# Kernel tuning notes

Hardware: AMD Instinct MI355X
Metric: run time of the kernel (lower is better)

Reference implementation:

```python
import jax, jax.numpy as jnp
import numpy as np

V, E, H = 50000, 300, 256  # vocab, word dim, per-direction hidden (nfeat_sent=2H=512)
B, T = 256, 64
NEG = -1e9


def _lstm_scan(x, mask, w_ih, w_hh, b):
    """x: [T,B,E], mask: [T,B,1] float. Masked steps keep (h,c) unchanged.
    Gate order matches torch.nn.LSTM: i, f, g, o."""
    Bsz = x.shape[1]
    Hd = w_hh.shape[1]
    init = (jnp.zeros((Bsz, Hd), x.dtype), jnp.zeros((Bsz, Hd), x.dtype))

    def step(carry, inp):
        h, c = carry
        xt, mt = inp
        z = xt @ w_ih.T + h @ w_hh.T + b  # [B,4H]
        i, f, g, o = jnp.split(z, 4, axis=-1)
        i = jax.nn.sigmoid(i); f = jax.nn.sigmoid(f)
        g = jnp.tanh(g); o = jax.nn.sigmoid(o)
        c_new = f * c + i * g
        h_new = o * jnp.tanh(c_new)
        c = mt * c_new + (1.0 - mt) * c
        h = mt * h_new + (1.0 - mt) * h
        return (h, c), h

    _, hs = jax.lax.scan(step, init, (x, mask))
    return hs  # [T,B,H]


def setup_inputs() -> dict:
    key = jax.random.key(0)
    ks = jax.random.split(key, 9)
    token_ids = jax.random.randint(ks[0], (B, T), 0, V, dtype=jnp.int32)
    lengths = jax.random.randint(ks[1], (B,), 1, T + 1, dtype=jnp.int32)
    emb = jax.random.normal(ks[2], (V, E), jnp.float32) * 0.1
    s = 0.05
    w_ih_f = jax.random.normal(ks[3], (4 * H, E), jnp.float32) * s
    w_hh_f = jax.random.normal(ks[4], (4 * H, H), jnp.float32) * s
    b_f = jax.random.normal(ks[5], (4 * H,), jnp.float32) * s  # b_ih + b_hh fused
    w_ih_b = jax.random.normal(ks[6], (4 * H, E), jnp.float32) * s
    w_hh_b = jax.random.normal(ks[7], (4 * H, H), jnp.float32) * s
    b_b = jax.random.normal(ks[8], (4 * H,), jnp.float32) * s
    return {"token_ids": token_ids, "lengths": lengths, "emb": emb,
            "w_ih_f": w_ih_f, "w_hh_f": w_hh_f, "b_f": b_f,
            "w_ih_b": w_ih_b, "w_hh_b": w_hh_b, "b_b": b_b}


def reference(token_ids, lengths, emb, w_ih_f, w_hh_f, b_f, w_ih_b, w_hh_b, b_b):
    # Batched equivalent of the per-sentence loop: embed -> biLSTM -> max over time.
    x = emb[token_ids]                              # [B,T,E]
    x = jnp.swapaxes(x, 0, 1)                       # [T,B,E] (time-major)
    valid = (jnp.arange(T)[:, None] < lengths[None, :])  # [T,B]
    mask = valid.astype(x.dtype)[:, :, None]        # [T,B,1]

    h_fwd = _lstm_scan(x, mask, w_ih_f, w_hh_f, b_f)  # [T,B,H]
    # Backward direction: reverse time; masked (pad) steps leave state at zero,
    # so each sentence's backward pass starts exactly at its last real token.
    h_bwd = _lstm_scan(x[::-1], mask[::-1], w_ih_b, w_hh_b, b_b)[::-1]

    out = jnp.concatenate([h_fwd, h_bwd], axis=-1)  # [T,B,2H]
    out = jnp.where(valid[:, :, None], out, NEG)
    return jnp.max(out, axis=0)                     # [B, 2H] == [B, nfeat_sent]
```

## Files before the change

kernel.cpp:

```cpp
#include <hip/hip_runtime.h>
#include <hip/hip_bf16.h>
#include <math.h>

#define VV 50000
#define EE 300
#define HD 256
#define BB 256
#define TT 64
#define NEGV -1e9f

#define OFF_H    0
#define OFF_C    262144
#define OFF_CTR  262144
#define OFF_B2   393216
#define OFF_WHHF 395264
#define OFF_WIHF 919552
#define WS_FULL_BYTES (1247232ULL * 4ULL)

typedef __attribute__((ext_vector_type(8))) short bf16x8;
typedef __attribute__((ext_vector_type(4))) float f32x4;

__device__ __forceinline__ float sigf(float x) {
  return 1.f / (1.f + __expf(-x));
}
__device__ __forceinline__ float tanhfast(float x) {
  return 1.f - 2.f / (__expf(2.f * x) + 1.f);
}
__device__ __forceinline__ unsigned short f2bf(float f) {
  union { float f; unsigned u; } x;
  x.f = f;
  unsigned r = x.u + 0x7fffu + ((x.u >> 16) & 1u);
  return (unsigned short)(r >> 16);
}

__global__ __launch_bounds__(256) void prep_all(
    const float* __restrict__ whf, const float* __restrict__ whb,
    const float* __restrict__ wif, const float* __restrict__ wib,
    const float* __restrict__ bf, const float* __restrict__ bb,
    float* __restrict__ ws) {
  int idx = blockIdx.x * 256 + threadIdx.x;
  if (idx < 131072) ws[OFF_H + idx] = 0.f;
  if (idx < 2048) {
    ((unsigned int*)(ws + OFF_CTR))[idx] = 0u;
    int dir = idx >> 10, jg = idx & 1023, j = jg >> 2, g = jg & 3;
    ws[OFF_B2 + idx] = (dir ? bb : bf)[g * HD + j];
  }
  if (idx < 65536) {
    int lane = idx & 63, kt = (idx >> 6) & 7, ngrp = (idx >> 9) & 63,
        dir = idx >> 15;
    int n = ngrp * 16 + (lane & 15);
    int j = n >> 2, g = n & 3;
    int k0 = kt * 32 + (lane >> 4) * 8;
    const float* W = dir ? whb : whf;
    const float* src = W + (size_t)((g << 8) + j) * HD + k0;
    union { unsigned short u[8]; uint4 q; } hp, lp;
#pragma unroll
    for (int e = 0; e < 8; ++e) {
      float v = src[e];
      unsigned short hh = f2bf(v);
      union { unsigned u; float f; } hf;
      hf.u = (unsigned)hh << 16;
      hp.u[e] = hh;
      lp.u[e] = f2bf(v - hf.f);
    }
    unsigned short* dst = (unsigned short*)(ws + OFF_WHHF) + (size_t)idx * 16;
    *(uint4*)dst = hp.q;
    *(uint4*)(dst + 8) = lp.q;
  }
  if (idx < 81920) {
    int lane = idx & 63;
    int f = idx >> 6;
    int kt = f % 10;
    int ngrp = (f / 10) & 63;
    int dir = f / 640;
    int n = ngrp * 16 + (lane & 15);
    int j = n >> 2, g = n & 3;
    int k0 = kt * 32 + (lane >> 4) * 8;
    const float* W = dir ? wib : wif;
    union { unsigned short u[8]; uint4 q; } p;
#pragma unroll
    for (int e = 0; e < 8; ++e) {
      int k = k0 + e;
      p.u[e] = (k < EE) ? f2bf(W[(size_t)((g << 8) + j) * EE + k])
                        : (unsigned short)0;
    }
    *(uint4*)((unsigned short*)(ws + OFF_WIHF) + (size_t)idx * 8) = p.q;
  }
}

__global__ __launch_bounds__(256) void init_kernel(float* __restrict__ ws,
                                                   float* __restrict__ out) {
  int idx = blockIdx.x * 256 + threadIdx.x;
  if (idx < 393216) ws[idx] = 0.f;
  if (idx < BB * 2 * HD) out[idx] = NEGV;
}

__global__ __launch_bounds__(512) void lstm_persist(
    const int* __restrict__ tok, const int* __restrict__ lens,
    const float* __restrict__ emb, float* __restrict__ ws,
    float* __restrict__ out) {
  const int bg = blockIdx.x;
  const int slice = blockIdx.y;
  const int dir = blockIdx.z;
  const int tid = threadIdx.x;
  const int lane = tid & 63;
  const int wv = tid >> 6;

  __shared__ __align__(16) unsigned short hfr[8192];
  __shared__ __align__(16) unsigned short ebuf[2][5120];
  __shared__ float z_sm[16][132];

  bf16x8 whi[8], wlo[8], wih[10];
  {
    const int ngrp = slice * 8 + wv;
    const unsigned short* p = (const unsigned short*)(ws + OFF_WHHF) +
                              (size_t)(((dir * 64 + ngrp) * 8) * 64 + lane) * 16;
#pragma unroll
    for (int kt = 0; kt < 8; ++kt) {
      whi[kt] = *(const bf16x8*)(p + kt * 1024);
      wlo[kt] = *(const bf16x8*)(p + kt * 1024 + 8);
    }
    const unsigned short* q = (const unsigned short*)(ws + OFF_WIHF) +
                              (size_t)(((dir * 64 + ngrp) * 10) * 64 + lane) * 8;
#pragma unroll
    for (int kt = 0; kt < 10; ++kt) wih[kt] = *(const bf16x8*)(q + kt * 512);
  }

  const int rg = tid >> 5;
  const int k8 = tid & 31;
  const int jl = tid & 31;
  const int brow = bg * 16 + rg;
  const int len = lens[brow];
  const int j = slice * 32 + jl;
  const float4 bias =
      *(const float4*)(ws + OFF_B2 + dir * 1024 + slice * 128 + jl * 4);
  unsigned int* ctr =
      (unsigned int*)(ws + OFF_CTR) + (size_t)(dir * 16 + bg) * 32;
  float* hb = ws + OFF_H;
  const int ld_r = lane & 15, ld_oct = lane >> 4;
  const int trow = brow * TT;
  const int o2 = 32 + (k8 & 7);
  const bool has2 = (k8 < 8);
  const int slot1 = (k8 >> 2) * 64 + rg * 4 + (k8 & 3);
  const int slot2 = ((o2 >> 2) * 64) + rg * 4 + (o2 & 3);

  float c = 0.f, omax = NEGV, h_prev = 0.f;

  {
    const int t0 = dir ? (TT - 1) : 0;
    const float* er = emb + (size_t)tok[trow + t0] * EE;
    float4 a0 = *(const float4*)(er + k8 * 8);
    float4 a1 = *(const float4*)(er + k8 * 8 + 4);
    union { unsigned short u[8]; uint4 q; } p;
    p.u[0] = f2bf(a0.x); p.u[1] = f2bf(a0.y); p.u[2] = f2bf(a0.z);
    p.u[3] = f2bf(a0.w); p.u[4] = f2bf(a1.x); p.u[5] = f2bf(a1.y);
    p.u[6] = f2bf(a1.z); p.u[7] = f2bf(a1.w);
    *(uint4*)&ebuf[0][slot1 * 8] = p.q;
    if (has2) {
      float4 b0 = make_float4(0.f, 0.f, 0.f, 0.f);
      float4 b1 = make_float4(0.f, 0.f, 0.f, 0.f);
      if (o2 <= 37) b0 = *(const float4*)(er + o2 * 8);
      if (o2 < 37) b1 = *(const float4*)(er + o2 * 8 + 4);
      union { unsigned short u[8]; uint4 q; } p2;
      p2.u[0] = f2bf(b0.x); p2.u[1] = f2bf(b0.y); p2.u[2] = f2bf(b0.z);
      p2.u[3] = f2bf(b0.w); p2.u[4] = f2bf(b1.x); p2.u[5] = f2bf(b1.y);
      p2.u[6] = f2bf(b1.z); p2.u[7] = f2bf(b1.w);
      *(uint4*)&ebuf[0][slot2 * 8] = p2.q;
    }
  }

  for (int s = 0; s < TT; ++s) {
    const int t = dir ? (TT - 1 - s) : s;
    const bool nstage = (s < TT - 1);
    const unsigned long long* s8 = (const unsigned long long*)(
        hb + (size_t)(((s & 1) * 2 + dir) * 256 + brow) * 256 + k8 * 8);
    unsigned long long u0 =
        __hip_atomic_load(s8 + 0, __ATOMIC_RELAXED, __HIP_MEMORY_SCOPE_AGENT);
    unsigned long long u1 =
        __hip_atomic_load(s8 + 1, __ATOMIC_RELAXED, __HIP_MEMORY_SCOPE_AGENT);
    unsigned long long u2 =
        __hip_atomic_load(s8 + 2, __ATOMIC_RELAXED, __HIP_MEMORY_SCOPE_AGENT);
    unsigned long long u3 =
        __hip_atomic_load(s8 + 3, __ATOMIC_RELAXED, __HIP_MEMORY_SCOPE_AGENT);
    float4 pe0, pe1, qe0, qe1;
    if (nstage) {
      const int tn = dir ? (TT - 2 - s) : (s + 1);
      const float* er = emb + (size_t)tok[trow + tn] * EE;
      pe0 = *(const float4*)(er + k8 * 8);
      pe1 = *(const float4*)(er + k8 * 8 + 4);
      qe0 = make_float4(0.f, 0.f, 0.f, 0.f);
      qe1 = make_float4(0.f, 0.f, 0.f, 0.f);
      if (has2) {
        if (o2 <= 37) qe0 = *(const float4*)(er + o2 * 8);
        if (o2 < 37) qe1 = *(const float4*)(er + o2 * 8 + 4);
      }
    }
    {
      float v[8];
      __builtin_memcpy(&v[0], &u0, 8);
      __builtin_memcpy(&v[2], &u1, 8);
      __builtin_memcpy(&v[4], &u2, 8);
      __builtin_memcpy(&v[6], &u3, 8);
      union { unsigned short u[8]; uint4 q; } hp, lp;
#pragma unroll
      for (int e = 0; e < 8; ++e) {
        unsigned short hh = f2bf(v[e]);
        union { unsigned u; float f; } hf;
        hf.u = (unsigned)hh << 16;
        hp.u[e] = hh;
        lp.u[e] = f2bf(v[e] - hf.f);
      }
      *(uint4*)&hfr[slot1 * 8] = hp.q;
      *(uint4*)&hfr[4096 + slot1 * 8] = lp.q;
    }
    __syncthreads();
    f32x4 acc[4];
#pragma unroll
    for (int i = 0; i < 4; ++i) {
      acc[i][0] = 0.f; acc[i][1] = 0.f; acc[i][2] = 0.f; acc[i][3] = 0.f;
    }
    const unsigned short* eb = ebuf[s & 1];
#pragma unroll
    for (int kt = 0; kt < 10; ++kt) {
      bf16x8 ax = *(const bf16x8*)(eb + (kt * 64 + ld_r * 4 + ld_oct) * 8);
      acc[kt & 3] =
          __builtin_amdgcn_mfma_f32_16x16x32_bf16(ax, wih[kt], acc[kt & 3], 0, 0, 0);
    }
#pragma unroll
    for (int kt = 0; kt < 8; ++kt) {
      const int sl = (kt * 64 + ld_r * 4 + ld_oct) * 8;
      bf16x8 ahi = *(const bf16x8*)(hfr + sl);
      bf16x8 alo = *(const bf16x8*)(hfr + 4096 + sl);
      f32x4 a = acc[kt & 3];
      a = __builtin_amdgcn_mfma_f32_16x16x32_bf16(ahi, whi[kt], a, 0, 0, 0);
      a = __builtin_amdgcn_mfma_f32_16x16x32_bf16(alo, whi[kt], a, 0, 0, 0);
      a = __builtin_amdgcn_mfma_f32_16x16x32_bf16(ahi, wlo[kt], a, 0, 0, 0);
      acc[kt & 3] = a;
    }
    f32x4 zf = (acc[0] + acc[1]) + (acc[2] + acc[3]);
#pragma unroll
    for (int i = 0; i < 4; ++i)
      z_sm[ld_oct * 4 + i][wv * 16 + ld_r] = zf[i];
    __syncthreads();
    const float4 z4 = *(const float4*)&z_sm[rg][jl * 4];
    float h_out = h_prev;
    if (t < len) {
      float ig = sigf(z4.x + bias.x);
      float fg = sigf(z4.y + bias.y);
      float gg = tanhfast(z4.z + bias.z);
      float og = sigf(z4.w + bias.w);
      c = fg * c + ig * gg;
      float hn = og * tanhfast(c);
      h_out = hn;
      omax = fmaxf(omax, hn);
    }
    h_prev = h_out;
    if (nstage) {
      float* dst =
          hb + (size_t)(((((s + 1) & 1) * 2 + dir) * 256) + brow) * 256 + j;
      __hip_atomic_store(dst, h_out, __ATOMIC_RELAXED,
                         __HIP_MEMORY_SCOPE_AGENT);
      unsigned short* ebn = ebuf[(s + 1) & 1];
      {
        union { unsigned short u[8]; uint4 q; } p;
        p.u[0] = f2bf(pe0.x); p.u[1] = f2bf(pe0.y); p.u[2] = f2bf(pe0.z);
        p.u[3] = f2bf(pe0.w); p.u[4] = f2bf(pe1.x); p.u[5] = f2bf(pe1.y);
        p.u[6] = f2bf(pe1.z); p.u[7] = f2bf(pe1.w);
        *(uint4*)&ebn[slot1 * 8] = p.q;
        if (has2) {
          union { unsigned short u[8]; uint4 q; } p2;
          p2.u[0] = f2bf(qe0.x); p2.u[1] = f2bf(qe0.y); p2.u[2] = f2bf(qe0.z);
          p2.u[3] = f2bf(qe0.w); p2.u[4] = f2bf(qe1.x); p2.u[5] = f2bf(qe1.y);
          p2.u[6] = f2bf(qe1.z); p2.u[7] = f2bf(qe1.w);
          *(uint4*)&ebn[slot2 * 8] = p2.q;
        }
      }
      asm volatile("s_waitcnt vmcnt(0)" ::: "memory");
      __syncthreads();
      if (tid == 0) {
        __hip_atomic_fetch_add(ctr, 1u, __ATOMIC_RELAXED,
                               __HIP_MEMORY_SCOPE_AGENT);
      }
      if (tid < 64) {
        const unsigned int target = 8u * (unsigned)(s + 1);
        while (__hip_atomic_load(ctr, __ATOMIC_RELAXED,
                                 __HIP_MEMORY_SCOPE_AGENT) < target) {
        }
      }
      __syncthreads();
      asm volatile("" ::: "memory");
    }
  }
  out[(size_t)brow * (2 * HD) + dir * HD + j] = omax;
}

__global__ __launch_bounds__(256) void step_fused(
    const int* __restrict__ tok, const int* __restrict__ lens,
    const float* __restrict__ emb,
    const float* __restrict__ wih_f, const float* __restrict__ whh_f,
    const float* __restrict__ bias_f,
    const float* __restrict__ wih_b, const float* __restrict__ whh_b,
    const float* __restrict__ bias_b,
    float* __restrict__ ws, float* __restrict__ out, int s) {
  const int tid = threadIdx.x;
  const int jt = blockIdx.x, bt = blockIdx.y, dir = blockIdx.z;
  const int j0 = jt * 32, b0g = bt * 16;
  const int t = (dir == 0) ? s : (TT - 1 - s);
  const float* Wih = dir ? wih_b : wih_f;
  const float* Whh = dir ? whh_b : whh_f;
  const float* bias = dir ? bias_b : bias_f;
  const float* hcur = ws + OFF_H + (size_t)((s & 1) * 2 + dir) * BB * HD;
  float* hnxt = ws + OFF_H + (size_t)(((s + 1) & 1) * 2 + dir) * BB * HD;
  float* cbuf = ws + OFF_C + (size_t)dir * BB * HD;

  __shared__ float a_sm[16][64];
  __shared__ float w_sm[64][132];
  __shared__ float z_sm[16][132];

  const int cg = tid & 31, bg = tid >> 5;
  float acc[2][4] = {{0.f, 0.f, 0.f, 0.f}, {0.f, 0.f, 0.f, 0.f}};

  for (int phase = 0; phase < 2; ++phase) {
    const float* W = phase ? Whh : Wih;
    const int K = phase ? HD : EE;
    for (int k0 = 0; k0 < K; k0 += 64) {
      const int klen = (K - k0) < 64 ? (K - k0) : 64;
      {
        int bl = tid >> 4, kk4 = tid & 15;
        if (kk4 * 4 < klen) {
          const float* src;
          if (phase == 0) {
            int tk = tok[(b0g + bl) * TT + t];
            src = emb + (size_t)tk * EE + k0 + kk4 * 4;
          } else {
            src = hcur + (size_t)(b0g + bl) * HD + k0 + kk4 * 4;
          }
          *(float4*)&a_sm[bl][kk4 * 4] = *(const float4*)src;
        }
      }
      for (int i = 0; i < 8; ++i) {
        int e = i * 256 + tid;
        int col = e >> 4, kk4 = e & 15;
        if (kk4 * 4 < klen) {
          int gcol = ((col >> 5) * HD) + j0 + (col & 31);
          float4 v = *(const float4*)(W + (size_t)gcol * K + k0 + kk4 * 4);
          w_sm[kk4 * 4 + 0][col] = v.x;
          w_sm[kk4 * 4 + 1][col] = v.y;
          w_sm[kk4 * 4 + 2][col] = v.z;
          w_sm[kk4 * 4 + 3][col] = v.w;
        }
      }
      __syncthreads();
      for (int k = 0; k < klen; ++k) {
        float a0 = a_sm[bg * 2 + 0][k];
        float a1 = a_sm[bg * 2 + 1][k];
        float4 w = *(const float4*)&w_sm[k][cg * 4];
        acc[0][0] += a0 * w.x; acc[0][1] += a0 * w.y;
        acc[0][2] += a0 * w.z; acc[0][3] += a0 * w.w;
        acc[1][0] += a1 * w.x; acc[1][1] += a1 * w.y;
        acc[1][2] += a1 * w.z; acc[1][3] += a1 * w.w;
      }
      __syncthreads();
    }
  }
  *(float4*)&z_sm[bg * 2 + 0][cg * 4] =
      make_float4(acc[0][0], acc[0][1], acc[0][2], acc[0][3]);
  *(float4*)&z_sm[bg * 2 + 1][cg * 4] =
      make_float4(acc[1][0], acc[1][1], acc[1][2], acc[1][3]);
  __syncthreads();
  for (int pi = 0; pi < 2; ++pi) {
    int p = pi * 256 + tid;
    int bl = p >> 5, jl = p & 31;
    int bglob = b0g + bl, jglob = j0 + jl;
    bool valid = t < lens[bglob];
    float h_old = hcur[(size_t)bglob * HD + jglob];
    float h_out = h_old;
    if (valid) {
      float zi = z_sm[bl][0 + jl] + bias[0 * HD + jglob];
      float zf = z_sm[bl][32 + jl] + bias[1 * HD + jglob];
      float zg = z_sm[bl][64 + jl] + bias[2 * HD + jglob];
      float zo = z_sm[bl][96 + jl] + bias[3 * HD + jglob];
      float ig = sigf(zi), fg = sigf(zf), gg = tanhf(zg), og = sigf(zo);
      float c_old = cbuf[(size_t)bglob * HD + jglob];
      float c_new = fg * c_old + ig * gg;
      float h_new = og * tanhf(c_new);
      cbuf[(size_t)bglob * HD + jglob] = c_new;
      h_out = h_new;
      float* op = out + (size_t)bglob * (2 * HD) + dir * HD + jglob;
      *op = fmaxf(*op, h_new);
    }
    hnxt[(size_t)bglob * HD + jglob] = h_out;
  }
}

extern "C" void kernel_launch(void* const* d_in, const int* in_sizes, int n_in,
                              void* d_out, int out_size, void* d_ws,
                              size_t ws_size, hipStream_t stream) {
  const int* tok = (const int*)d_in[0];
  const int* lens = (const int*)d_in[1];
  const float* emb = (const float*)d_in[2];
  const float* wih_f = (const float*)d_in[3];
  const float* whh_f = (const float*)d_in[4];
  const float* b_f = (const float*)d_in[5];
  const float* wih_b = (const float*)d_in[6];
  const float* whh_b = (const float*)d_in[7];
  const float* b_b = (const float*)d_in[8];
  float* out = (float*)d_out;
  float* ws = (float*)d_ws;

  const bool full = ws_size >= WS_FULL_BYTES;
  if (full) {
    hipLaunchKernelGGL(prep_all, dim3(512), dim3(256), 0, stream, whh_f,
                       whh_b, wih_f, wih_b, b_f, b_b, ws);
    hipLaunchKernelGGL(lstm_persist, dim3(16, 8, 2), dim3(512), 0, stream,
                       tok, lens, emb, ws, out);
  } else {
    hipLaunchKernelGGL(init_kernel, dim3(1536), dim3(256), 0, stream, ws, out);
    for (int s = 0; s < TT; ++s) {
      hipLaunchKernelGGL(step_fused, dim3(8, 16, 2), dim3(256), 0, stream, tok,
                         lens, emb, wih_f, whh_f, b_f, wih_b, whh_b, b_b, ws,
                         out, s);
    }
  }
}
```

Measured before the change: 220.3 us.

## Exchange hidden state as pre-split bf16 fragments and replace LDS gate transpose with shuffles

The producer now writes the hidden state to global memory already split into bf16 hi/lo pairs in the MFMA fragment layout. Consumers can copy it straight into LDS without per-step conversion. The gate results are regrouped across lanes with xor-shuffles instead of a z_sm shared-memory round trip, which removes one __syncthreads per step. The cost is two 16-bit scattered atomic stores per element instead of one float store, plus a larger workspace layout.

```diff
diff --git a/kernel.cpp b/kernel.cpp
--- a/kernel.cpp
+++ b/kernel.cpp
@@ -9,13 +9,14 @@
 #define TT 64
 #define NEGV -1e9f
 
-#define OFF_H    0
-#define OFF_C    262144
-#define OFF_CTR  262144
-#define OFF_B2   393216
-#define OFF_WHHF 395264
-#define OFF_WIHF 919552
-#define WS_FULL_BYTES (1247232ULL * 4ULL)
+#define OFF_HF   0
+#define OFF_CTR  524288
+#define OFF_B2   526336
+#define OFF_WHHF 528384
+#define OFF_WIHF 1052672
+#define WS_FULL_BYTES (1380352ULL * 4ULL)
+#define FB_H 0
+#define FB_C 262144
 
 typedef __attribute__((ext_vector_type(8))) short bf16x8;
 typedef __attribute__((ext_vector_type(4))) float f32x4;
@@ -39,7 +40,7 @@
     const float* __restrict__ bf, const float* __restrict__ bb,
     float* __restrict__ ws) {
   int idx = blockIdx.x * 256 + threadIdx.x;
-  if (idx < 131072) ws[OFF_H + idx] = 0.f;
+  if (idx < 131072) ws[OFF_HF + idx] = 0.f;
   if (idx < 2048) {
     ((unsigned int*)(ws + OFF_CTR))[idx] = 0u;
     int dir = idx >> 10, jg = idx & 1023, j = jg >> 2, g = jg & 3;
@@ -106,13 +107,12 @@
   const int lane = tid & 63;
   const int wv = tid >> 6;
 
-  __shared__ __align__(16) unsigned short hfr[8192];
+  __shared__ __align__(16) unsigned short hfr[2][512][8];
   __shared__ __align__(16) unsigned short ebuf[2][5120];
-  __shared__ float z_sm[16][132];
 
   bf16x8 whi[8], wlo[8], wih[10];
+  const int ngrp = slice * 8 + wv;
   {
-    const int ngrp = slice * 8 + wv;
     const unsigned short* p = (const unsigned short*)(ws + OFF_WHHF) +
                               (size_t)(((dir * 64 + ngrp) * 8) * 64 + lane) * 16;
 #pragma unroll
@@ -128,27 +128,35 @@
 
   const int rg = tid >> 5;
   const int k8 = tid & 31;
-  const int jl = tid & 31;
-  const int brow = bg * 16 + rg;
-  const int len = lens[brow];
-  const int j = slice * 32 + jl;
-  const float4 bias =
-      *(const float4*)(ws + OFF_B2 + dir * 1024 + slice * 128 + jl * 4);
-  unsigned int* ctr =
-      (unsigned int*)(ws + OFF_CTR) + (size_t)(dir * 16 + bg) * 32;
-  float* hb = ws + OFF_H;
-  const int ld_r = lane & 15, ld_oct = lane >> 4;
-  const int trow = brow * TT;
+  const int stage_row = bg * 16 + rg;
+  const int strow = stage_row * TT;
   const int o2 = 32 + (k8 & 7);
   const bool has2 = (k8 < 8);
   const int slot1 = (k8 >> 2) * 64 + rg * 4 + (k8 & 3);
   const int slot2 = ((o2 >> 2) * 64) + rg * 4 + (o2 & 3);
 
+  const int q = lane & 3;
+  const int base = lane & 12;
+  const int r = (lane >> 4) * 4 + q;
+  const int gate_row = bg * 16 + r;
+  const int len = lens[gate_row];
+  const int jloc = ngrp * 4 + (base >> 2);
+  const float4 bias4 =
+      *(const float4*)(ws + OFF_B2 + dir * 1024 + ngrp * 16 + base);
+  const int slot_j = (jloc >> 5) * 64 + r * 4 + ((jloc >> 3) & 3);
+  const int e_j = jloc & 7;
+
+  const int ld_slot = (lane & 15) * 4 + (lane >> 4);
+
+  unsigned int* ctr =
+      (unsigned int*)(ws + OFF_CTR) + (size_t)(dir * 16 + bg) * 32;
+  unsigned short* hfg = (unsigned short*)(ws + OFF_HF);
+
   float c = 0.f, omax = NEGV, h_prev = 0.f;
 
   {
     const int t0 = dir ? (TT - 1) : 0;
-    const float* er = emb + (size_t)tok[trow + t0] * EE;
+    const float* er = emb + (size_t)tok[strow + t0] * EE;
     float4 a0 = *(const float4*)(er + k8 * 8);
     float4 a1 = *(const float4*)(er + k8 * 8 + 4);
     union { unsigned short u[8]; uint4 q; } p;
@@ -172,20 +180,24 @@
   for (int s = 0; s < TT; ++s) {
     const int t = dir ? (TT - 1 - s) : s;
     const bool nstage = (s < TT - 1);
-    const unsigned long long* s8 = (const unsigned long long*)(
-        hb + (size_t)(((s & 1) * 2 + dir) * 256 + brow) * 256 + k8 * 8);
-    unsigned long long u0 =
-        __hip_atomic_load(s8 + 0, __ATOMIC_RELAXED, __HIP_MEMORY_SCOPE_AGENT);
-    unsigned long long u1 =
-        __hip_atomic_load(s8 + 1, __ATOMIC_RELAXED, __HIP_MEMORY_SCOPE_AGENT);
-    unsigned long long u2 =
-        __hip_atomic_load(s8 + 2, __ATOMIC_RELAXED, __HIP_MEMORY_SCOPE_AGENT);
-    unsigned long long u3 =
-        __hip_atomic_load(s8 + 3, __ATOMIC_RELAXED, __HIP_MEMORY_SCOPE_AGENT);
+    const unsigned long long* hsrc = (const unsigned long long*)(
+        hfg + (size_t)(((s & 1) * 2 + dir) * 16 + bg) * 8192);
+    unsigned long long hu0 = __hip_atomic_load(hsrc + tid * 4 + 0,
+                                               __ATOMIC_RELAXED,
+                                               __HIP_MEMORY_SCOPE_AGENT);
+    unsigned long long hu1 = __hip_atomic_load(hsrc + tid * 4 + 1,
+                                               __ATOMIC_RELAXED,
+                                               __HIP_MEMORY_SCOPE_AGENT);
+    unsigned long long hu2 = __hip_atomic_load(hsrc + tid * 4 + 2,
+                                               __ATOMIC_RELAXED,
+                                               __HIP_MEMORY_SCOPE_AGENT);
+    unsigned long long hu3 = __hip_atomic_load(hsrc + tid * 4 + 3,
+                                               __ATOMIC_RELAXED,
+                                               __HIP_MEMORY_SCOPE_AGENT);
     float4 pe0, pe1, qe0, qe1;
     if (nstage) {
       const int tn = dir ? (TT - 2 - s) : (s + 1);
-      const float* er = emb + (size_t)tok[trow + tn] * EE;
+      const float* er = emb + (size_t)tok[strow + tn] * EE;
       pe0 = *(const float4*)(er + k8 * 8);
       pe1 = *(const float4*)(er + k8 * 8 + 4);
       qe0 = make_float4(0.f, 0.f, 0.f, 0.f);
@@ -196,22 +208,11 @@
       }
     }
     {
-      float v[8];
-      __builtin_memcpy(&v[0], &u0, 8);
-      __builtin_memcpy(&v[2], &u1, 8);
-      __builtin_memcpy(&v[4], &u2, 8);
-      __builtin_memcpy(&v[6], &u3, 8);
-      union { unsigned short u[8]; uint4 q; } hp, lp;
-#pragma unroll
-      for (int e = 0; e < 8; ++e) {
-        unsigned short hh = f2bf(v[e]);
-        union { unsigned u; float f; } hf;
-        hf.u = (unsigned)hh << 16;
-        hp.u[e] = hh;
-        lp.u[e] = f2bf(v[e] - hf.f);
-      }
-      *(uint4*)&hfr[slot1 * 8] = hp.q;
-      *(uint4*)&hfr[4096 + slot1 * 8] = lp.q;
+      unsigned long long* hdst_l = (unsigned long long*)hfr;
+      hdst_l[tid * 4 + 0] = hu0;
+      hdst_l[tid * 4 + 1] = hu1;
+      hdst_l[tid * 4 + 2] = hu2;
+      hdst_l[tid * 4 + 3] = hu3;
     }
     __syncthreads();
     f32x4 acc[4];
@@ -222,15 +223,14 @@
     const unsigned short* eb = ebuf[s & 1];
 #pragma unroll
     for (int kt = 0; kt < 10; ++kt) {
-      bf16x8 ax = *(const bf16x8*)(eb + (kt * 64 + ld_r * 4 + ld_oct) * 8);
+      bf16x8 ax = *(const bf16x8*)(eb + (kt * 64 + ld_slot) * 8);
       acc[kt & 3] =
           __builtin_amdgcn_mfma_f32_16x16x32_bf16(ax, wih[kt], acc[kt & 3], 0, 0, 0);
     }
 #pragma unroll
     for (int kt = 0; kt < 8; ++kt) {
-      const int sl = (kt * 64 + ld_r * 4 + ld_oct) * 8;
-      bf16x8 ahi = *(const bf16x8*)(hfr + sl);
-      bf16x8 alo = *(const bf16x8*)(hfr + 4096 + sl);
+      bf16x8 ahi = *(const bf16x8*)&hfr[0][kt * 64 + ld_slot][0];
+      bf16x8 alo = *(const bf16x8*)&hfr[1][kt * 64 + ld_slot][0];
       f32x4 a = acc[kt & 3];
       a = __builtin_amdgcn_mfma_f32_16x16x32_bf16(ahi, whi[kt], a, 0, 0, 0);
       a = __builtin_amdgcn_mfma_f32_16x16x32_bf16(alo, whi[kt], a, 0, 0, 0);
@@ -238,17 +238,29 @@
       acc[kt & 3] = a;
     }
     f32x4 zf = (acc[0] + acc[1]) + (acc[2] + acc[3]);
-#pragma unroll
-    for (int i = 0; i < 4; ++i)
-      z_sm[ld_oct * 4 + i][wv * 16 + ld_r] = zf[i];
-    __syncthreads();
-    const float4 z4 = *(const float4*)&z_sm[rg][jl * 4];
+    float v0 = zf[0], v1 = zf[1], v2 = zf[2], v3 = zf[3];
+    {
+      float s0 = __shfl_xor(v1, 1), s1 = __shfl_xor(v0, 1);
+      float s2 = __shfl_xor(v3, 1), s3 = __shfl_xor(v2, 1);
+      const bool qb = (q & 1) != 0;
+      float a0 = qb ? s0 : v0;
+      float a1 = qb ? v1 : s1;
+      float a2 = qb ? s2 : v2;
+      float a3 = qb ? v3 : s3;
+      float t0 = __shfl_xor(a2, 2), t1 = __shfl_xor(a3, 2);
+      float t2 = __shfl_xor(a0, 2), t3 = __shfl_xor(a1, 2);
+      const bool q2 = (q & 2) != 0;
+      v0 = q2 ? t0 : a0;
+      v1 = q2 ? t1 : a1;
+      v2 = q2 ? a2 : t2;
+      v3 = q2 ? a3 : t3;
+    }
     float h_out = h_prev;
     if (t < len) {
-      float ig = sigf(z4.x + bias.x);
-      float fg = sigf(z4.y + bias.y);
-      float gg = tanhfast(z4.z + bias.z);
-      float og = sigf(z4.w + bias.w);
+      float ig = sigf(v0 + bias4.x);
+      float fg = sigf(v1 + bias4.y);
+      float gg = tanhfast(v2 + bias4.z);
+      float og = sigf(v3 + bias4.w);
       c = fg * c + ig * gg;
       float hn = og * tanhfast(c);
       h_out = hn;
@@ -256,9 +268,15 @@
     }
     h_prev = h_out;
     if (nstage) {
-      float* dst =
-          hb + (size_t)(((((s + 1) & 1) * 2 + dir) * 256) + brow) * 256 + j;
-      __hip_atomic_store(dst, h_out, __ATOMIC_RELAXED,
+      unsigned short hi = f2bf(h_out);
+      union { unsigned u; float f; } hf;
+      hf.u = (unsigned)hi << 16;
+      unsigned short lo = f2bf(h_out - hf.f);
+      unsigned short* hdst =
+          hfg + (size_t)((((s + 1) & 1) * 2 + dir) * 16 + bg) * 8192;
+      __hip_atomic_store(hdst + slot_j * 8 + e_j, hi, __ATOMIC_RELAXED,
+                         __HIP_MEMORY_SCOPE_AGENT);
+      __hip_atomic_store(hdst + 4096 + slot_j * 8 + e_j, lo, __ATOMIC_RELAXED,
                          __HIP_MEMORY_SCOPE_AGENT);
       unsigned short* ebn = ebuf[(s + 1) & 1];
       {
@@ -291,7 +309,7 @@
       asm volatile("" ::: "memory");
     }
   }
-  out[(size_t)brow * (2 * HD) + dir * HD + j] = omax;
+  out[(size_t)gate_row * (2 * HD) + dir * HD + jloc] = omax;
 }
 
 __global__ __launch_bounds__(256) void step_fused(
@@ -309,15 +327,15 @@
   const float* Wih = dir ? wih_b : wih_f;
   const float* Whh = dir ? whh_b : whh_f;
   const float* bias = dir ? bias_b : bias_f;
-  const float* hcur = ws + OFF_H + (size_t)((s & 1) * 2 + dir) * BB * HD;
-  float* hnxt = ws + OFF_H + (size_t)(((s + 1) & 1) * 2 + dir) * BB * HD;
-  float* cbuf = ws + OFF_C + (size_t)dir * BB * HD;
+  const float* hcur = ws + FB_H + (size_t)((s & 1) * 2 + dir) * BB * HD;
+  float* hnxt = ws + FB_H + (size_t)(((s + 1) & 1) * 2 + dir) * BB * HD;
+  float* cbuf = ws + FB_C + (size_t)dir * BB * HD;
 
   __shared__ float a_sm[16][64];
   __shared__ float w_sm[64][132];
   __shared__ float z_sm[16][132];
 
-  const int cg = tid & 31, bg = tid >> 5;
+  const int cg = tid & 31, bgr = tid >> 5;
   float acc[2][4] = {{0.f, 0.f, 0.f, 0.f}, {0.f, 0.f, 0.f, 0.f}};
 
   for (int phase = 0; phase < 2; ++phase) {
@@ -352,8 +370,8 @@
       }
       __syncthreads();
       for (int k = 0; k < klen; ++k) {
-        float a0 = a_sm[bg * 2 + 0][k];
-        float a1 = a_sm[bg * 2 + 1][k];
+        float a0 = a_sm[bgr * 2 + 0][k];
+        float a1 = a_sm[bgr * 2 + 1][k];
         float4 w = *(const float4*)&w_sm[k][cg * 4];
         acc[0][0] += a0 * w.x; acc[0][1] += a0 * w.y;
         acc[0][2] += a0 * w.z; acc[0][3] += a0 * w.w;
@@ -363,9 +381,9 @@
       __syncthreads();
     }
   }
-  *(float4*)&z_sm[bg * 2 + 0][cg * 4] =
+  *(float4*)&z_sm[bgr * 2 + 0][cg * 4] =
       make_float4(acc[0][0], acc[0][1], acc[0][2], acc[0][3]);
-  *(float4*)&z_sm[bg * 2 + 1][cg * 4] =
+  *(float4*)&z_sm[bgr * 2 + 1][cg * 4] =
       make_float4(acc[1][0], acc[1][1], acc[1][2], acc[1][3]);
   __syncthreads();
   for (int pi = 0; pi < 2; ++pi) {
```

Result: slower. 229.1 us (+4.0%).
